# Performance work log

Hardware: AMD Instinct MI355X
Metric: run time of the kernel (lower is better)

Reference implementation:

```python
import jax, jax.numpy as jnp
import numpy as np

H, HD = 8, 64  # num_heads, head_dim
EPS = 1e-6

def rmsnorm(x, scale):
    return x * jax.lax.rsqrt(jnp.mean(x * x, axis=-1, keepdims=True) + EPS) * scale

def lecun(key, shape):
    fan_in = shape[0]
    return jax.random.normal(key, shape, dtype=jnp.float32) * (fan_in ** -0.5)

def setup_inputs() -> dict:
    key = jax.random.key(0)
    ks = jax.random.split(key, 12)
    B, S, D = 2, 512, 512
    hidden = H * HD            # 512
    ffn = 4 * D                # 2048
    return {
        "inputs": jax.random.normal(ks[0], (B, S, D), dtype=jnp.float32),
        "mask": jnp.zeros((B, S), dtype=jnp.float32),
        "carry": jnp.zeros((B, H, HD, HD), dtype=jnp.float32),
        "ln1": jnp.ones((D,), dtype=jnp.float32),
        "Wq": lecun(ks[1], (D, hidden)),
        "Wk": lecun(ks[2], (D, hidden)),
        "Wv": lecun(ks[3], (D, hidden)),
        "attn_ln": jnp.ones((hidden,), dtype=jnp.float32),
        "Wo": lecun(ks[4], (hidden, D)),
        "bo": jnp.zeros((D,), dtype=jnp.float32),
        "ln2": jnp.ones((D,), dtype=jnp.float32),
        "Wg": lecun(ks[5], (D, ffn)),
        "Wu": lecun(ks[6], (D, ffn)),
        "Wd": lecun(ks[7], (ffn, D)),
    }

def reference(inputs, mask, carry, ln1, Wq, Wk, Wv, attn_ln, Wo, bo, ln2, Wg, Wu, Wd):
    B, S, D = inputs.shape
    skip = inputs
    x = rmsnorm(inputs, ln1)
    # projections + relu feature map
    q = jax.nn.relu((x @ Wq).reshape(B, S, H, HD))
    k = jax.nn.relu((x @ Wk).reshape(B, S, H, HD))
    v = (x @ Wv).reshape(B, S, H, HD)
    # matrix-valued state update: Bmat_t = v_t k_t^T  [B,S,H,HD,HD]
    Bmat = v[..., :, None] * k[..., None, :]
    # decay: identity, zeroed where mask==1 (episode reset)
    m = mask[:, :, None, None, None]
    A = jnp.broadcast_to(jnp.eye(HD, dtype=x.dtype), Bmat.shape) * (1.0 - m)

    def binop(lhs, rhs):
        a_i, b_i = lhs
        a_j, b_j = rhs
        return jnp.matmul(a_i, a_j), jnp.matmul(b_i, a_j) + b_j

    cum_decay, hidden_states = jax.lax.associative_scan(binop, (A, Bmat), axis=1)
    # fold in incoming carry
    states = jnp.matmul(carry[:, None], cum_decay) + hidden_states  # [B,S,H,HD,HD]
    attn = jnp.matmul(states, q[..., None]).squeeze(-1).reshape(B, S, H * HD)
    attn = rmsnorm(attn, attn_ln)
    y = attn @ Wo + bo
    final_carry = states[:, -1]
    # residual + SwiGLU FFN
    x = y + skip
    skip2 = x
    x = rmsnorm(x, ln2)
    x = (jax.nn.silu(x @ Wg) * (x @ Wu)) @ Wd
    return (final_carry, x + skip2)
```

## Files before the change

kernel.cpp:

```cpp
#include <hip/hip_runtime.h>
#include <math.h>

typedef __bf16 bf16x8 __attribute__((ext_vector_type(8)));
typedef float  f32x4  __attribute__((ext_vector_type(4)));

constexpr int B_=2, S_=512, D_=512, H_=8, HD_=64, FFN_=2048, NC_=8;
constexpr float EPS_=1e-6f;

__device__ __forceinline__ __bf16 f2bf(float f){
    union{float f;unsigned u;}x; x.f=f;
    unsigned r=(x.u+0x7fffu+((x.u>>16)&1u))>>16;
    union{unsigned short s;__bf16 b;}y; y.s=(unsigned short)r; return y.b;
}
__device__ __forceinline__ float bf2f(unsigned short s){
    union{unsigned u;float f;}x; x.u=((unsigned)s)<<16; return x.f;
}
__device__ __forceinline__ void bf8_f32(uint4 p, float* o){
    unsigned w[4]={p.x,p.y,p.z,p.w};
#pragma unroll
    for(int i=0;i<4;i++){ o[2*i]=bf2f((unsigned short)(w[i]&0xffffu)); o[2*i+1]=bf2f((unsigned short)(w[i]>>16)); }
}
__device__ __forceinline__ f32x4 MF(bf16x8 a, bf16x8 b, f32x4 c){
    return __builtin_amdgcn_mfma_f32_16x16x32_bf16(a,b,c,0,0,0);
}
#define GLOAD16(g,l) __builtin_amdgcn_global_load_lds((__attribute__((address_space(1))) const void*)(g),(__attribute__((address_space(3))) void*)(l),16,0,0)

__device__ __forceinline__ void rowsq_atomic(float* accb, int row0, int lane, float p[4]){
#pragma unroll
    for(int r=0;r<4;r++){
        float v = p[r];
        v += __shfl_xor(v, 1, 64);
        v += __shfl_xor(v, 2, 64);
        v += __shfl_xor(v, 4, 64);
        v += __shfl_xor(v, 8, 64);
        if((lane&15)==0) atomicAdd(accb + row0 + r, v);
    }
}

__global__ __launch_bounds__(256) void prep_k(const float* __restrict__ Wg,
    const float* __restrict__ Wu, const float* __restrict__ Wd,
    const float* __restrict__ Wq, const float* __restrict__ Wk,
    const float* __restrict__ Wv, const float* __restrict__ Wo,
    __bf16* __restrict__ WT, const float* __restrict__ inputs,
    float* __restrict__ rs1, float* __restrict__ rs2acc, float* __restrict__ rs3acc){
    __shared__ __bf16 s[64][72];
    int t = blockIdx.x, tid = threadIdx.x;
    if(t >= 1024){
        int row = (t-1024)*4 + (tid>>6), lane = tid&63;
        const float4* p = (const float4*)(inputs + (size_t)row*D_) + lane*2;
        float4 a=p[0], b=p[1];
        float ss = a.x*a.x+a.y*a.y+a.z*a.z+a.w*a.w + b.x*b.x+b.y*b.y+b.z*b.z+b.w*b.w;
        for(int off=32; off>0; off>>=1) ss += __shfl_down(ss, off, 64);
        if(lane==0) rs1[row] = rsqrtf(ss/(float)D_ + EPS_);
        float4 z = {0.f,0.f,0.f,0.f};
        if(t==1024) ((float4*)rs2acc)[tid] = z;
        if(t==1025) ((float4*)rs3acc)[tid] = z;
        return;
    }
    const float* src; __bf16* dst; int K,N,lt;
    if      (t<256){ src=Wg; dst=WT;          K=512;  N=2048; lt=t; }
    else if (t<512){ src=Wu; dst=WT+1048576;  K=512;  N=2048; lt=t-256; }
    else if (t<768){ src=Wd; dst=WT+2097152;  K=2048; N=512;  lt=t-512; }
    else if (t<832){ src=Wq; dst=WT+3145728;  K=512;  N=512;  lt=t-768; }
    else if (t<896){ src=Wk; dst=WT+3407872;  K=512;  N=512;  lt=t-832; }
    else if (t<960){ src=Wv; dst=WT+3670016;  K=512;  N=512;  lt=t-896; }
    else           { src=Wo; dst=WT+3932160;  K=512;  N=512;  lt=t-960; }
    int nt64 = N>>6, tk = lt/nt64, tn = lt%nt64;
    {
        int jk = tid>>2, jn0 = (tid&3)*16;
        const float* p = src + (size_t)(tk*64+jk)*N + tn*64 + jn0;
        float4 a0=((const float4*)p)[0], a1=((const float4*)p)[1],
               a2=((const float4*)p)[2], a3=((const float4*)p)[3];
        bf16x8 w0, w1;
        w0[0]=f2bf(a0.x); w0[1]=f2bf(a0.y); w0[2]=f2bf(a0.z); w0[3]=f2bf(a0.w);
        w0[4]=f2bf(a1.x); w0[5]=f2bf(a1.y); w0[6]=f2bf(a1.z); w0[7]=f2bf(a1.w);
        w1[0]=f2bf(a2.x); w1[1]=f2bf(a2.y); w1[2]=f2bf(a2.z); w1[3]=f2bf(a2.w);
        w1[4]=f2bf(a3.x); w1[5]=f2bf(a3.y); w1[6]=f2bf(a3.z); w1[7]=f2bf(a3.w);
        *(bf16x8*)&s[jk][jn0] = w0; *(bf16x8*)&s[jk][jn0+8] = w1;
    }
    __syncthreads();
    {
        int jn = tid&63, jkq = (tid>>6)*16;
        bf16x8 w0, w1;
#pragma unroll
        for(int j=0;j<8;j++){ w0[j]=s[jkq+j][jn]; w1[j]=s[jkq+8+j][jn]; }
        __bf16* q = dst + (size_t)(tn*64+jn)*K + tk*64 + jkq;
        *(bf16x8*)q = w0; *(bf16x8*)(q+8) = w1;
    }
}

__device__ __forceinline__ void stageB1(const __bf16* __restrict__ Bt, int n0, int K, int kk,
                                        __bf16* sB0, __bf16* sB1, int wave, int lane){
    int row = (wave<<4) + (lane>>2), kq = (lane&3)<<3;
    const __bf16* g = Bt + (size_t)(n0+row)*K + kk + kq;
    GLOAD16(g,      sB0 + (wave<<9));
    GLOAD16(g + 32, sB1 + (wave<<9));
}
struct ARf { float4 a0,a1,a2,a3, g0,g1,g2,g3; };
__device__ __forceinline__ ARf loadA_f32(const float* __restrict__ A, const float* __restrict__ g,
                                         int m0, int K, int kk, int tid){
    int row = tid>>2, kq = (tid&3)<<4;
    const float4* p = (const float4*)(A + (size_t)(m0+row)*K + kk + kq);
    const float4* gp = (const float4*)(g + kk + kq);
    ARf o;
    o.a0=p[0]; o.a1=p[1]; o.a2=p[2]; o.a3=p[3];
    o.g0=gp[0]; o.g1=gp[1]; o.g2=gp[2]; o.g3=gp[3];
    return o;
}
__device__ __forceinline__ void writeA_f32(const ARf& o, float r, __bf16* sA0, __bf16* sA1, int tid){
    int row = tid>>2, kq = (tid&3)<<4;
    bf16x8 w0, w1;
    w0[0]=f2bf(o.a0.x*r*o.g0.x); w0[1]=f2bf(o.a0.y*r*o.g0.y);
    w0[2]=f2bf(o.a0.z*r*o.g0.z); w0[3]=f2bf(o.a0.w*r*o.g0.w);
    w0[4]=f2bf(o.a1.x*r*o.g1.x); w0[5]=f2bf(o.a1.y*r*o.g1.y);
    w0[6]=f2bf(o.a1.z*r*o.g1.z); w0[7]=f2bf(o.a1.w*r*o.g1.w);
    w1[0]=f2bf(o.a2.x*r*o.g2.x); w1[1]=f2bf(o.a2.y*r*o.g2.y);
    w1[2]=f2bf(o.a2.z*r*o.g2.z); w1[3]=f2bf(o.a2.w*r*o.g2.w);
    w1[4]=f2bf(o.a3.x*r*o.g3.x); w1[5]=f2bf(o.a3.y*r*o.g3.y);
    w1[6]=f2bf(o.a3.z*r*o.g3.z); w1[7]=f2bf(o.a3.w*r*o.g3.w);
    __bf16* d = (kq<32) ? (sA0 + row*32 + kq) : (sA1 + row*32 + kq-32);
    *(bf16x8*)d = w0; *(bf16x8*)(d+8) = w1;
}
struct ARb { uint4 p0,p1; float4 g0,g1,g2,g3; };
__device__ __forceinline__ ARb loadA_bf16(const __bf16* __restrict__ A, const float* __restrict__ g,
                                          int m0, int K, int kk, int tid){
    int row = tid>>2, kq = (tid&3)<<4;
    const __bf16* p = A + (size_t)(m0+row)*K + kk + kq;
    const float4* gp = (const float4*)(g + kk + kq);
    ARb o;
    o.p0 = *(const uint4*)p; o.p1 = *(const uint4*)(p+8);
    o.g0=gp[0]; o.g1=gp[1]; o.g2=gp[2]; o.g3=gp[3];
    return o;
}
__device__ __forceinline__ void writeA_bf16(const ARb& o, float r, __bf16* sA0, __bf16* sA1, int tid){
    int row = tid>>2, kq = (tid&3)<<4;
    float v[16]; bf8_f32(o.p0, v); bf8_f32(o.p1, v+8);
    float gf[16] = {o.g0.x,o.g0.y,o.g0.z,o.g0.w, o.g1.x,o.g1.y,o.g1.z,o.g1.w,
                    o.g2.x,o.g2.y,o.g2.z,o.g2.w, o.g3.x,o.g3.y,o.g3.z,o.g3.w};
    bf16x8 w0, w1;
#pragma unroll
    for(int j=0;j<8;j++){ w0[j]=f2bf(v[j]*r*gf[j]); w1[j]=f2bf(v[8+j]*r*gf[8+j]); }
    __bf16* d = (kq<32) ? (sA0 + row*32 + kq) : (sA1 + row*32 + kq-32);
    *(bf16x8*)d = w0; *(bf16x8*)(d+8) = w1;
}
__device__ __forceinline__ void mfma_tile(const __bf16* sA0, const __bf16* sA1,
        const __bf16* sB0, const __bf16* sB1, int wave, int lane, f32x4 acc[4]){
    int ar = (((wave<<4)+(lane&15))<<5) + ((lane>>4)<<3);
    bf16x8 a0 = *(const bf16x8*)(sA0+ar);
    bf16x8 a1 = *(const bf16x8*)(sA1+ar);
#pragma unroll
    for(int nt=0;nt<4;nt++){
        int br = (((nt<<4)+(lane&15))<<5) + ((lane>>4)<<3);
        acc[nt] = MF(a0, *(const bf16x8*)(sB0+br), acc[nt]);
        acc[nt] = MF(a1, *(const bf16x8*)(sB1+br), acc[nt]);
    }
}

__global__ __launch_bounds__(256) void gemm_qkv_k(const float* __restrict__ in,
        const float* __restrict__ rs1, const float* __restrict__ ln1,
        const __bf16* __restrict__ Bt, __bf16* __restrict__ Qb,
        __bf16* __restrict__ Kb, __bf16* __restrict__ Vb){
    __shared__ __bf16 sA0[2][2048], sA1[2][2048], sB0[2][2048], sB1[2][2048];
    int tid=threadIdx.x, wave=tid>>6, lane=tid&63;
    int n0 = blockIdx.x*64, m0 = blockIdx.y*64;
    float r = rs1[m0+(tid>>2)];
    f32x4 acc[4] = {};
    {
        ARf a = loadA_f32(in, ln1, m0, 512, 0, tid);
        stageB1(Bt, n0, 512, 0, sB0[0], sB1[0], wave, lane);
        writeA_f32(a, r, sA0[0], sA1[0], tid);
        __syncthreads();
    }
    int cur = 0;
#pragma unroll
    for(int it=0; it<8; ++it){
        int nxt = cur^1;
        ARf a;
        if(it<7){
            a = loadA_f32(in, ln1, m0, 512, (it+1)*64, tid);
            stageB1(Bt, n0, 512, (it+1)*64, sB0[nxt], sB1[nxt], wave, lane);
        }
        mfma_tile(sA0[cur],sA1[cur],sB0[cur],sB1[cur],wave,lane,acc);
        if(it<7) writeA_f32(a, r, sA0[nxt], sA1[nxt], tid);
        __syncthreads();
        cur = nxt;
    }
    int seg = n0>>9, nc = n0&511;
    __bf16* Out = seg==0 ? Qb : (seg==1 ? Kb : Vb);
    bool rl = seg<2;
    int r0 = (wave<<4) + ((lane>>4)<<2);
#pragma unroll
    for(int nt=0;nt<4;nt++){
        int col = nc + nt*16 + (lane&15);
#pragma unroll
        for(int rr=0;rr<4;rr++){
            float v = acc[nt][rr]; if(rl) v = fmaxf(v,0.f);
            Out[(size_t)(m0+r0+rr)*512 + col] = f2bf(v);
        }
    }
}

__global__ __launch_bounds__(256) void scanA_k(const __bf16* __restrict__ Kb,
        const __bf16* __restrict__ Vb, const float* __restrict__ mask,
        __bf16* __restrict__ MS, float* __restrict__ Pws){
    int bid = blockIdx.x;
    int c = bid&7, h = (bid>>3)&7, b = bid>>6;
    __shared__ __bf16 sKT0[2048], sKT1[2048], sVT0[2048], sVT1[2048];
    __shared__ float scv[64], ssp[64];
    int tid = threadIdx.x, wave = tid>>6, lane = tid&63;
    const __bf16* Kg = Kb + (size_t)(b*512 + c*64)*512 + h*64;
    const __bf16* Vg = Vb + (size_t)(b*512 + c*64)*512 + h*64;
    if(tid<64) scv[tid] = 1.f - mask[b*512 + c*64 + tid];
    __syncthreads();
    if(tid==0){
        float sp = 1.f;
        for(int t=63;t>=0;--t){ ssp[t]=sp; sp*=scv[t]; }
        Pws[bid] = sp;
    }
    __syncthreads();
#pragma unroll
    for(int p=0;p<2;p++){
        int t = (tid>>3) + p*32, i0 = (tid&7)*8;
        uint4 kr = *(const uint4*)(Kg + (size_t)t*512 + i0);
        uint4 vr = *(const uint4*)(Vg + (size_t)t*512 + i0);
        const __bf16* kp = (const __bf16*)&kr;
        const unsigned short* vp = (const unsigned short*)&vr;
        float sp = ssp[t];
        __bf16* kh = p ? sKT1 : sKT0;
        __bf16* vh = p ? sVT1 : sVT0;
#pragma unroll
        for(int j=0;j<8;j++){
            kh[(i0+j)*32 + (t&31)] = kp[j];
            vh[(i0+j)*32 + (t&31)] = f2bf(bf2f(vp[j])*sp);
        }
    }
    __syncthreads();
    f32x4 am[4] = {};
    mfma_tile(sVT0, sVT1, sKT0, sKT1, wave, lane, am);
    __bf16* Mo = MS + (size_t)bid*4096;
    int r0 = (wave<<4) + ((lane>>4)<<2);
#pragma unroll
    for(int nt=0;nt<4;nt++){
        int j = nt*16 + (lane&15);
#pragma unroll
        for(int r=0;r<4;r++) Mo[(size_t)(r0+r)*64 + j] = f2bf(am[nt][r]);
    }
}

__global__ __launch_bounds__(256) void scanC_k(const __bf16* __restrict__ Qb,
        const __bf16* __restrict__ Kb, const __bf16* __restrict__ Vb,
        const float* __restrict__ mask, const __bf16* __restrict__ MS,
        const float* __restrict__ carry, const float* __restrict__ Pws,
        float* __restrict__ carry_out, __bf16* __restrict__ attn,
        float* __restrict__ rs2acc){
    int bid = blockIdx.x;
    int c = bid&7, h = (bid>>3)&7, b = bid>>6;
    int bh = b*H_ + h;
    __shared__ __bf16 sQ0[2048], sQ1[2048], sK0[2048], sK1[2048];
    __shared__ __bf16 sS0[2048], sS1[2048];
    __shared__ __bf16 sVT0[2048], sVT1[2048];
    __shared__ __bf16 sW0[2048], sW1[2048];
    __shared__ float Wtab[64][64];
    __shared__ float scv[64], pp[64];
    int tid = threadIdx.x, wave = tid>>6, lane = tid&63;
    const __bf16* Qg = Qb + (size_t)(b*512 + c*64)*512 + h*64;
    const __bf16* Kg = Kb + (size_t)(b*512 + c*64)*512 + h*64;
    const __bf16* Vg = Vb + (size_t)(b*512 + c*64)*512 + h*64;

    stageB1(Qg, 0, 512, 0, sQ0, sQ1, wave, lane);
    stageB1(Kg, 0, 512, 0, sK0, sK1, wave, lane);
    if(tid<64) scv[tid] = 1.f - mask[b*512 + c*64 + tid];
#pragma unroll
    for(int p=0;p<2;p++){
        int u = (tid>>3) + p*32, i0 = (tid&7)*8;
        uint4 vr = *(const uint4*)(Vg + (size_t)u*512 + i0);
        const __bf16* vp = (const __bf16*)&vr;
        __bf16* vh = p ? sVT1 : sVT0;
#pragma unroll
        for(int j=0;j<8;j++) vh[(i0+j)*32 + (u&31)] = vp[j];
    }
    {
        int i = tid>>2, j0 = (tid&3)*16;
        float s[16];
        const float4* c4 = (const float4*)(carry + (size_t)bh*4096 + i*64 + j0);
        float4 s4[4] = {c4[0],c4[1],c4[2],c4[3]};
        float* sp = (float*)s4;
#pragma unroll
        for(int j=0;j<16;j++) s[j]=sp[j];
        for(int cc=0; cc<c; ++cc){
            float P = Pws[bh*8+cc];
            const __bf16* mp = MS + ((size_t)bh*8+cc)*4096 + i*64 + j0;
            float mv[16]; bf8_f32(*(const uint4*)mp, mv); bf8_f32(*(const uint4*)(mp+8), mv+8);
#pragma unroll
            for(int j=0;j<16;j++) s[j] = s[j]*P + mv[j];
        }
        bf16x8 w0, w1;
#pragma unroll
        for(int j=0;j<8;j++){ w0[j]=f2bf(s[j]); w1[j]=f2bf(s[8+j]); }
        __bf16* d = (j0<32) ? (sS0 + i*32 + j0) : (sS1 + i*32 + j0-32);
        *(bf16x8*)d = w0; *(bf16x8*)(d+8) = w1;
        if(c==7){
            float P = Pws[bh*8+7];
            const __bf16* mp = MS + ((size_t)bh*8+7)*4096 + i*64 + j0;
            float mv[16]; bf8_f32(*(const uint4*)mp, mv); bf8_f32(*(const uint4*)(mp+8), mv+8);
            float4 o4[4];
            float* ov = (float*)o4;
#pragma unroll
            for(int j=0;j<16;j++) ov[j] = s[j]*P + mv[j];
            float4* co = (float4*)(carry_out + (size_t)bh*4096 + i*64 + j0);
            co[0]=o4[0]; co[1]=o4[1]; co[2]=o4[2]; co[3]=o4[3];
        }
    }
    __syncthreads();
    if(tid<64){
        int u = tid; float w = 1.f;
        for(int t=0;t<64;t++){
            if(t>u) w *= scv[t];
            Wtab[u][t] = (t<u) ? 0.f : w;
        }
    }
    if(tid==64){
        float p=1.f;
        for(int t=0;t<64;t++){ p*=scv[t]; pp[t]=p; }
    }
    f32x4 sc[4] = {};
    mfma_tile(sK0, sK1, sQ0, sQ1, wave, lane, sc);
    __syncthreads();
    {
        int u0 = (wave<<4) + ((lane>>4)<<2);
#pragma unroll
        for(int nt=0;nt<4;nt++){
            int t = nt*16 + (lane&15);
#pragma unroll
            for(int r=0;r<4;r++){
                int u = u0 + r;
                float v = sc[nt][r] * Wtab[u][t];
                ((u<32) ? sW0 : sW1)[t*32 + (u&31)] = f2bf(v);
            }
        }
    }
    __syncthreads();
    f32x4 aI[4] = {}, aX[4] = {};
    mfma_tile(sW0, sW1, sVT0, sVT1, wave, lane, aI);
    mfma_tile(sQ0, sQ1, sS0, sS1, wave, lane, aX);
    int t0 = (wave<<4) + ((lane>>4)<<2);
    float psum[4] = {0.f,0.f,0.f,0.f};
#pragma unroll
    for(int nt=0;nt<4;nt++){
        int i = nt*16 + (lane&15);
#pragma unroll
        for(int r=0;r<4;r++){
            int t = t0 + r;
            float o = aI[nt][r] + aX[nt][r]*pp[t];
            attn[(size_t)(b*512 + c*64 + t)*512 + h*64 + i] = f2bf(o);
            psum[r] += o*o;
        }
    }
    rowsq_atomic(rs2acc, b*512 + c*64 + t0, lane, psum);
}

__global__ __launch_bounds__(256) void gemm_wo_k(const __bf16* __restrict__ attn,
        const float* __restrict__ rs2acc, const float* __restrict__ aln,
        const __bf16* __restrict__ Bt, const float* __restrict__ bo,
        const float* __restrict__ skip, float* __restrict__ outx,
        __bf16* __restrict__ X1, float* __restrict__ rs3acc){
    __shared__ __bf16 sA0[2][2048], sA1[2][2048], sB0[2][2048], sB1[2][2048];
    int tid=threadIdx.x, wave=tid>>6, lane=tid&63;
    int n0 = blockIdx.x*64, m0 = blockIdx.y*64;
    float r = rsqrtf(rs2acc[m0+(tid>>2)]*(1.f/(float)D_) + EPS_);
    f32x4 acc[4] = {};
    {
        ARb a = loadA_bf16(attn, aln, m0, 512, 0, tid);
        stageB1(Bt, n0, 512, 0, sB0[0], sB1[0], wave, lane);
        writeA_bf16(a, r, sA0[0], sA1[0], tid);
        __syncthreads();
    }
    int cur = 0;
#pragma unroll
    for(int it=0; it<8; ++it){
        int nxt = cur^1;
        ARb a;
        if(it<7){
            a = loadA_bf16(attn, aln, m0, 512, (it+1)*64, tid);
            stageB1(Bt, n0, 512, (it+1)*64, sB0[nxt], sB1[nxt], wave, lane);
        }
        mfma_tile(sA0[cur],sA1[cur],sB0[cur],sB1[cur],wave,lane,acc);
        if(it<7) writeA_bf16(a, r, sA0[nxt], sA1[nxt], tid);
        __syncthreads();
        cur = nxt;
    }
    int r0 = (wave<<4) + ((lane>>4)<<2);
    float psum[4] = {0.f,0.f,0.f,0.f};
#pragma unroll
    for(int nt=0;nt<4;nt++){
        int col = n0 + nt*16 + (lane&15);
#pragma unroll
        for(int rr=0;rr<4;rr++){
            int row = m0+r0+rr;
            float v = acc[nt][rr] + bo[col] + skip[(size_t)row*512+col];
            outx[(size_t)row*512+col] = v;
            X1[(size_t)row*512+col] = f2bf(v);
            psum[rr] += v*v;
        }
    }
    rowsq_atomic(rs3acc, m0+r0, lane, psum);
}

__global__ __launch_bounds__(256) void gemm_dual_k(const __bf16* __restrict__ X1,
        const float* __restrict__ rs3acc, const float* __restrict__ ln2,
        const __bf16* __restrict__ Gt, const __bf16* __restrict__ Ut,
        __bf16* __restrict__ Hb){
    __shared__ __bf16 sA0[2][2048], sA1[2][2048];
    __shared__ __bf16 sG0[2][2048], sG1[2][2048], sU0[2][2048], sU1[2][2048];
    int tid=threadIdx.x, wave=tid>>6, lane=tid&63;
    int n0 = blockIdx.x*64, m0 = blockIdx.y*64;
    float r = rsqrtf(rs3acc[m0+(tid>>2)]*(1.f/(float)D_) + EPS_);
    f32x4 ag[4] = {}, au[4] = {};
    {
        ARb a = loadA_bf16(X1, ln2, m0, 512, 0, tid);
        stageB1(Gt, n0, 512, 0, sG0[0], sG1[0], wave, lane);
        stageB1(Ut, n0, 512, 0, sU0[0], sU1[0], wave, lane);
        writeA_bf16(a, r, sA0[0], sA1[0], tid);
        __syncthreads();
    }
    int cur = 0;
#pragma unroll
    for(int it=0; it<8; ++it){
        int nxt = cur^1;
        ARb a;
        if(it<7){
            a = loadA_bf16(X1, ln2, m0, 512, (it+1)*64, tid);
            stageB1(Gt, n0, 512, (it+1)*64, sG0[nxt], sG1[nxt], wave, lane);
            stageB1(Ut, n0, 512, (it+1)*64, sU0[nxt], sU1[nxt], wave, lane);
        }
        {
            int ar = (((wave<<4)+(lane&15))<<5) + ((lane>>4)<<3);
            bf16x8 a0 = *(const bf16x8*)(sA0[cur]+ar);
            bf16x8 a1 = *(const bf16x8*)(sA1[cur]+ar);
#pragma unroll
            for(int nt=0;nt<4;nt++){
                int br = (((nt<<4)+(lane&15))<<5) + ((lane>>4)<<3);
                ag[nt] = MF(a0, *(const bf16x8*)(sG0[cur]+br), ag[nt]);
                ag[nt] = MF(a1, *(const bf16x8*)(sG1[cur]+br), ag[nt]);
                au[nt] = MF(a0, *(const bf16x8*)(sU0[cur]+br), au[nt]);
                au[nt] = MF(a1, *(const bf16x8*)(sU1[cur]+br), au[nt]);
            }
        }
        if(it<7) writeA_bf16(a, r, sA0[nxt], sA1[nxt], tid);
        __syncthreads();
        cur = nxt;
    }
    int r0 = (wave<<4) + ((lane>>4)<<2);
#pragma unroll
    for(int nt=0;nt<4;nt++){
        int col = n0 + nt*16 + (lane&15);
#pragma unroll
        for(int rr=0;rr<4;rr++){
            float gv = ag[nt][rr], uv = au[nt][rr];
            float hv = (gv / (1.f + __expf(-gv))) * uv;
            Hb[(size_t)(m0+r0+rr)*FFN_ + col] = f2bf(hv);
        }
    }
}

__global__ __launch_bounds__(256) void gemm_wd_k(const __bf16* __restrict__ Hb,
        const __bf16* __restrict__ Bt, float* __restrict__ outx){
    __shared__ __bf16 sA0[2][2048], sA1[2][2048], sB0[2][2048], sB1[2][2048];
    int tid=threadIdx.x, wave=tid>>6, lane=tid&63;
    int n0 = blockIdx.x*64, m0 = blockIdx.y*64, ks = blockIdx.z*512;
    f32x4 acc[4] = {};
    int row = (wave<<4) + (lane>>2), kq = (lane&3)<<3;
    {
        stageB1(Bt, n0, FFN_, ks, sB0[0], sB1[0], wave, lane);
        const __bf16* g = Hb + (size_t)(m0+row)*FFN_ + ks + kq;
        GLOAD16(g,      sA0[0] + (wave<<9));
        GLOAD16(g + 32, sA1[0] + (wave<<9));
        __syncthreads();
    }
    int cur = 0;
#pragma unroll
    for(int it=0; it<8; ++it){
        int nxt = cur^1;
        if(it<7){
            int kk = ks + (it+1)*64;
            stageB1(Bt, n0, FFN_, kk, sB0[nxt], sB1[nxt], wave, lane);
            const __bf16* g = Hb + (size_t)(m0+row)*FFN_ + kk + kq;
            GLOAD16(g,      sA0[nxt] + (wave<<9));
            GLOAD16(g + 32, sA1[nxt] + (wave<<9));
        }
        mfma_tile(sA0[cur],sA1[cur],sB0[cur],sB1[cur],wave,lane,acc);
        __syncthreads();
        cur = nxt;
    }
    int r0 = (wave<<4) + ((lane>>4)<<2);
#pragma unroll
    for(int nt=0;nt<4;nt++){
        int col = n0 + nt*16 + (lane&15);
#pragma unroll
        for(int r=0;r<4;r++)
            atomicAdd(&outx[(size_t)(m0+r0+r)*512 + col], acc[nt][r]);
    }
}

extern "C" void kernel_launch(void* const* d_in, const int* in_sizes, int n_in,
                              void* d_out, int out_size, void* d_ws, size_t ws_size,
                              hipStream_t stream) {
    const float* inputs  = (const float*)d_in[0];
    const float* mask    = (const float*)d_in[1];
    const float* carry   = (const float*)d_in[2];
    const float* ln1     = (const float*)d_in[3];
    const float* Wq      = (const float*)d_in[4];
    const float* Wk      = (const float*)d_in[5];
    const float* Wv      = (const float*)d_in[6];
    const float* attn_ln = (const float*)d_in[7];
    const float* Wo      = (const float*)d_in[8];
    const float* bo      = (const float*)d_in[9];
    const float* ln2     = (const float*)d_in[10];
    const float* Wg      = (const float*)d_in[11];
    const float* Wu      = (const float*)d_in[12];
    const float* Wd      = (const float*)d_in[13];

    float* out_carry = (float*)d_out;
    float* out_x     = (float*)d_out + 65536;

    __bf16* wb = (__bf16*)d_ws;
    float*  wf = (float*)d_ws;
    __bf16* WgT   = wb;
    __bf16* WuT   = wb + 1048576;
    __bf16* WdT   = wb + 2097152;
    __bf16* WqkvT = wb + 3145728;
    __bf16* WoT   = wb + 3932160;
    __bf16* Qb    = wb + 4194304;
    __bf16* Kb    = wb + 4718592;
    __bf16* Vb    = wb + 5242880;
    __bf16* Hb    = wb + 3145728;
    __bf16* MS    = wb + 5767168;
    float*  Pws   = wf + 3145728;
    float*  rs1   = wf + 3145856;
    float*  rs2a  = wf + 3146880;
    float*  rs3a  = wf + 3147904;

    prep_k<<<dim3(1280), dim3(256), 0, stream>>>(Wg,Wu,Wd,Wq,Wk,Wv,Wo, wb, inputs, rs1, rs2a, rs3a);
    gemm_qkv_k<<<dim3(24,16), dim3(256), 0, stream>>>(inputs, rs1, ln1, WqkvT, Qb, Kb, Vb);
    scanA_k<<<dim3(128), dim3(256), 0, stream>>>(Kb, Vb, mask, MS, Pws);
    scanC_k<<<dim3(128), dim3(256), 0, stream>>>(Qb, Kb, Vb, mask, MS, carry, Pws, out_carry, Qb, rs2a);
    gemm_wo_k<<<dim3(8,16), dim3(256), 0, stream>>>(Qb, rs2a, attn_ln, WoT, bo, inputs, out_x, Vb, rs3a);
    gemm_dual_k<<<dim3(32,16), dim3(256), 0, stream>>>(Vb, rs3a, ln2, WgT, WuT, Hb);
    gemm_wd_k<<<dim3(8,16,4), dim3(256), 0, stream>>>(Hb, WdT, out_x);
}
```

Before: 161.7 us.

## Fuse chunked scan into one sequential kernel, coalesce epilogue stores, drop split-K atomics

The two-pass chunked scan (per-chunk state kernel plus prefix kernel) is replaced by a single kernel with one block per batch-head that walks the 8 chunks in order and keeps the running state in registers. That removes a launch and the intermediate state buffer, but only 16 blocks run instead of 128. Several GEMM epilogues now stage results in shared memory and write coalesced 16-byte stores. The Wd GEMM drops its 4-way split-K with atomics for one 32-step K loop per tile, which gives fewer blocks and a longer serial loop.

```diff
diff --git a/kernel.cpp b/kernel.cpp
--- a/kernel.cpp
+++ b/kernel.cpp
@@ -188,175 +188,173 @@
     int seg = n0>>9, nc = n0&511;
     __bf16* Out = seg==0 ? Qb : (seg==1 ? Kb : Vb);
     bool rl = seg<2;
+    __bf16* tile = &sA0[0][0];
     int r0 = (wave<<4) + ((lane>>4)<<2);
 #pragma unroll
     for(int nt=0;nt<4;nt++){
-        int col = nc + nt*16 + (lane&15);
+        int col = nt*16 + (lane&15);
 #pragma unroll
         for(int rr=0;rr<4;rr++){
             float v = acc[nt][rr]; if(rl) v = fmaxf(v,0.f);
-            Out[(size_t)(m0+r0+rr)*512 + col] = f2bf(v);
-        }
-    }
-}
-
-__global__ __launch_bounds__(256) void scanA_k(const __bf16* __restrict__ Kb,
-        const __bf16* __restrict__ Vb, const float* __restrict__ mask,
-        __bf16* __restrict__ MS, float* __restrict__ Pws){
-    int bid = blockIdx.x;
-    int c = bid&7, h = (bid>>3)&7, b = bid>>6;
-    __shared__ __bf16 sKT0[2048], sKT1[2048], sVT0[2048], sVT1[2048];
-    __shared__ float scv[64], ssp[64];
-    int tid = threadIdx.x, wave = tid>>6, lane = tid&63;
-    const __bf16* Kg = Kb + (size_t)(b*512 + c*64)*512 + h*64;
-    const __bf16* Vg = Vb + (size_t)(b*512 + c*64)*512 + h*64;
-    if(tid<64) scv[tid] = 1.f - mask[b*512 + c*64 + tid];
-    __syncthreads();
-    if(tid==0){
-        float sp = 1.f;
-        for(int t=63;t>=0;--t){ ssp[t]=sp; sp*=scv[t]; }
-        Pws[bid] = sp;
+            tile[(r0+rr)*64 + col] = f2bf(v);
+        }
     }
     __syncthreads();
 #pragma unroll
     for(int p=0;p<2;p++){
-        int t = (tid>>3) + p*32, i0 = (tid&7)*8;
-        uint4 kr = *(const uint4*)(Kg + (size_t)t*512 + i0);
-        uint4 vr = *(const uint4*)(Vg + (size_t)t*512 + i0);
-        const __bf16* kp = (const __bf16*)&kr;
-        const unsigned short* vp = (const unsigned short*)&vr;
-        float sp = ssp[t];
-        __bf16* kh = p ? sKT1 : sKT0;
-        __bf16* vh = p ? sVT1 : sVT0;
-#pragma unroll
-        for(int j=0;j<8;j++){
-            kh[(i0+j)*32 + (t&31)] = kp[j];
-            vh[(i0+j)*32 + (t&31)] = f2bf(bf2f(vp[j])*sp);
-        }
-    }
-    __syncthreads();
-    f32x4 am[4] = {};
-    mfma_tile(sVT0, sVT1, sKT0, sKT1, wave, lane, am);
-    __bf16* Mo = MS + (size_t)bid*4096;
-    int r0 = (wave<<4) + ((lane>>4)<<2);
-#pragma unroll
-    for(int nt=0;nt<4;nt++){
-        int j = nt*16 + (lane&15);
-#pragma unroll
-        for(int r=0;r<4;r++) Mo[(size_t)(r0+r)*64 + j] = f2bf(am[nt][r]);
-    }
-}
-
-__global__ __launch_bounds__(256) void scanC_k(const __bf16* __restrict__ Qb,
+        int row = (tid>>3) + p*32, c0 = (tid&7)*8;
+        *(uint4*)(Out + (size_t)(m0+row)*512 + nc + c0) = *(const uint4*)&tile[row*64 + c0];
+    }
+}
+
+__global__ __launch_bounds__(256) void scan_k(const __bf16* __restrict__ Qb,
         const __bf16* __restrict__ Kb, const __bf16* __restrict__ Vb,
-        const float* __restrict__ mask, const __bf16* __restrict__ MS,
-        const float* __restrict__ carry, const float* __restrict__ Pws,
+        const float* __restrict__ mask, const float* __restrict__ carry,
         float* __restrict__ carry_out, __bf16* __restrict__ attn,
         float* __restrict__ rs2acc){
-    int bid = blockIdx.x;
-    int c = bid&7, h = (bid>>3)&7, b = bid>>6;
-    int bh = b*H_ + h;
-    __shared__ __bf16 sQ0[2048], sQ1[2048], sK0[2048], sK1[2048];
-    __shared__ __bf16 sS0[2048], sS1[2048];
-    __shared__ __bf16 sVT0[2048], sVT1[2048];
-    __shared__ __bf16 sW0[2048], sW1[2048];
+    int bh = blockIdx.x, h = bh & 7, b = bh >> 3;
+    __shared__ __bf16 sQ[4096], sK[4096], sKT[4096], sVT[4096], sS[4096], sW[4096];
     __shared__ float Wtab[64][64];
-    __shared__ float scv[64], pp[64];
+    __shared__ float scv[64], ssp[64], pp[64];
+    __shared__ float Psh;
     int tid = threadIdx.x, wave = tid>>6, lane = tid&63;
-    const __bf16* Qg = Qb + (size_t)(b*512 + c*64)*512 + h*64;
-    const __bf16* Kg = Kb + (size_t)(b*512 + c*64)*512 + h*64;
-    const __bf16* Vg = Vb + (size_t)(b*512 + c*64)*512 + h*64;
-
-    stageB1(Qg, 0, 512, 0, sQ0, sQ1, wave, lane);
-    stageB1(Kg, 0, 512, 0, sK0, sK1, wave, lane);
-    if(tid<64) scv[tid] = 1.f - mask[b*512 + c*64 + tid];
-#pragma unroll
-    for(int p=0;p<2;p++){
-        int u = (tid>>3) + p*32, i0 = (tid&7)*8;
-        uint4 vr = *(const uint4*)(Vg + (size_t)u*512 + i0);
-        const __bf16* vp = (const __bf16*)&vr;
-        __bf16* vh = p ? sVT1 : sVT0;
-#pragma unroll
-        for(int j=0;j<8;j++) vh[(i0+j)*32 + (u&31)] = vp[j];
-    }
-    {
-        int i = tid>>2, j0 = (tid&3)*16;
-        float s[16];
-        const float4* c4 = (const float4*)(carry + (size_t)bh*4096 + i*64 + j0);
-        float4 s4[4] = {c4[0],c4[1],c4[2],c4[3]};
-        float* sp = (float*)s4;
-#pragma unroll
-        for(int j=0;j<16;j++) s[j]=sp[j];
-        for(int cc=0; cc<c; ++cc){
-            float P = Pws[bh*8+cc];
-            const __bf16* mp = MS + ((size_t)bh*8+cc)*4096 + i*64 + j0;
-            float mv[16]; bf8_f32(*(const uint4*)mp, mv); bf8_f32(*(const uint4*)(mp+8), mv+8);
-#pragma unroll
-            for(int j=0;j<16;j++) s[j] = s[j]*P + mv[j];
-        }
-        bf16x8 w0, w1;
-#pragma unroll
-        for(int j=0;j<8;j++){ w0[j]=f2bf(s[j]); w1[j]=f2bf(s[8+j]); }
-        __bf16* d = (j0<32) ? (sS0 + i*32 + j0) : (sS1 + i*32 + j0-32);
-        *(bf16x8*)d = w0; *(bf16x8*)(d+8) = w1;
-        if(c==7){
-            float P = Pws[bh*8+7];
-            const __bf16* mp = MS + ((size_t)bh*8+7)*4096 + i*64 + j0;
-            float mv[16]; bf8_f32(*(const uint4*)mp, mv); bf8_f32(*(const uint4*)(mp+8), mv+8);
-            float4 o4[4];
-            float* ov = (float*)o4;
-#pragma unroll
-            for(int j=0;j<16;j++) ov[j] = s[j]*P + mv[j];
-            float4* co = (float4*)(carry_out + (size_t)bh*4096 + i*64 + j0);
-            co[0]=o4[0]; co[1]=o4[1]; co[2]=o4[2]; co[3]=o4[3];
-        }
-    }
-    __syncthreads();
-    if(tid<64){
-        int u = tid; float w = 1.f;
-        for(int t=0;t<64;t++){
-            if(t>u) w *= scv[t];
-            Wtab[u][t] = (t<u) ? 0.f : w;
-        }
-    }
-    if(tid==64){
-        float p=1.f;
-        for(int t=0;t<64;t++){ p*=scv[t]; pp[t]=p; }
-    }
-    f32x4 sc[4] = {};
-    mfma_tile(sK0, sK1, sQ0, sQ1, wave, lane, sc);
-    __syncthreads();
-    {
-        int u0 = (wave<<4) + ((lane>>4)<<2);
+    int r0 = (wave<<4) + ((lane>>4)<<2);
+    int jc = lane & 15;
+
+#pragma unroll
+    for(int p=0;p<4;p++){
+        int fi = tid + p*256;
+        int row = fi>>4, c4 = (fi&15)*4;
+        *(float4*)&Wtab[row][c4] = *(const float4*)(carry + (size_t)bh*4096 + row*64 + c4);
+    }
+    __syncthreads();
+    f32x4 S[4];
+#pragma unroll
+    for(int nt=0;nt<4;nt++)
+#pragma unroll
+        for(int rr=0;rr<4;rr++) S[nt][rr] = Wtab[r0+rr][nt*16+jc];
+    __syncthreads();
+
+    for(int c=0; c<NC_; ++c){
+        const __bf16* Qg = Qb + (size_t)(b*512 + c*64)*512 + h*64;
+        const __bf16* Kg = Kb + (size_t)(b*512 + c*64)*512 + h*64;
+        const __bf16* Vg = Vb + (size_t)(b*512 + c*64)*512 + h*64;
+        stageB1(Qg, 0, 512, 0, sQ, sQ+2048, wave, lane);
+        stageB1(Kg, 0, 512, 0, sK, sK+2048, wave, lane);
+        uint4 kv[2], vv[2];
+#pragma unroll
+        for(int p=0;p<2;p++){
+            int u = (tid>>3) + p*32, i0 = (tid&7)*8;
+            kv[p] = *(const uint4*)(Kg + (size_t)u*512 + i0);
+            vv[p] = *(const uint4*)(Vg + (size_t)u*512 + i0);
+        }
+        if(tid<64) scv[tid] = 1.f - mask[b*512 + c*64 + tid];
 #pragma unroll
         for(int nt=0;nt<4;nt++){
-            int t = nt*16 + (lane&15);
-#pragma unroll
-            for(int r=0;r<4;r++){
-                int u = u0 + r;
-                float v = sc[nt][r] * Wtab[u][t];
-                ((u<32) ? sW0 : sW1)[t*32 + (u&31)] = f2bf(v);
+            int j = nt*16 + jc;
+            __bf16* half = (j<32) ? sS : sS+2048;
+#pragma unroll
+            for(int rr=0;rr<4;rr++) half[(r0+rr)*32 + (j&31)] = f2bf(S[nt][rr]);
+        }
+        __syncthreads();
+        if(tid==0){
+            float sp=1.f;
+            for(int t=63;t>=0;--t){ ssp[t]=sp; sp*=scv[t]; }
+            Psh = sp;
+        }
+        if(tid==64){
+            float p=1.f;
+            for(int t=0;t<64;t++){ p*=scv[t]; pp[t]=p; }
+        }
+        if(tid<64){
+            int u=tid; float w=1.f;
+            for(int t=0;t<64;t++){ if(t>u) w*=scv[t]; Wtab[u][t]=(t<u)?0.f:w; }
+        }
+#pragma unroll
+        for(int p=0;p<2;p++){
+            int u = (tid>>3) + p*32, i0 = (tid&7)*8;
+            const __bf16* vp = (const __bf16*)&vv[p];
+            __bf16* vh = (i0<32)? sVT : sVT;
+#pragma unroll
+            for(int j=0;j<8;j++){
+                int i = i0+j;
+                ((i<32)? sVT : sVT+2048)[0];
+                ((u<32)? sVT : sVT+2048)[i*32 + (u&31)] = vp[j];
             }
         }
-    }
-    __syncthreads();
-    f32x4 aI[4] = {}, aX[4] = {};
-    mfma_tile(sW0, sW1, sVT0, sVT1, wave, lane, aI);
-    mfma_tile(sQ0, sQ1, sS0, sS1, wave, lane, aX);
-    int t0 = (wave<<4) + ((lane>>4)<<2);
-    float psum[4] = {0.f,0.f,0.f,0.f};
-#pragma unroll
-    for(int nt=0;nt<4;nt++){
-        int i = nt*16 + (lane&15);
-#pragma unroll
-        for(int r=0;r<4;r++){
-            int t = t0 + r;
-            float o = aI[nt][r] + aX[nt][r]*pp[t];
-            attn[(size_t)(b*512 + c*64 + t)*512 + h*64 + i] = f2bf(o);
-            psum[r] += o*o;
-        }
-    }
-    rowsq_atomic(rs2acc, b*512 + c*64 + t0, lane, psum);
+        __syncthreads();
+#pragma unroll
+        for(int p=0;p<2;p++){
+            int u = (tid>>3) + p*32, i0 = (tid&7)*8;
+            const unsigned short* kp = (const unsigned short*)&kv[p];
+            float sp = ssp[u];
+#pragma unroll
+            for(int j=0;j<8;j++){
+                int jj = i0+j;
+                ((u<32)? sKT : sKT+2048)[jj*32 + (u&31)] = f2bf(bf2f(kp[j])*sp);
+            }
+        }
+        __syncthreads();
+        f32x4 sc[4] = {}, aM[4] = {}, aX[4] = {};
+        mfma_tile(sK, sK+2048, sQ, sQ+2048, wave, lane, sc);
+        mfma_tile(sVT, sVT+2048, sKT, sKT+2048, wave, lane, aM);
+        mfma_tile(sQ, sQ+2048, sS, sS+2048, wave, lane, aX);
+#pragma unroll
+        for(int nt=0;nt<4;nt++){
+            int t = nt*16 + jc;
+#pragma unroll
+            for(int rr=0;rr<4;rr++){
+                int u = r0 + rr;
+                float v = sc[nt][rr] * Wtab[u][t];
+                ((u<32)? sW : sW+2048)[t*32 + (u&31)] = f2bf(v);
+            }
+        }
+        __syncthreads();
+        f32x4 aI[4] = {};
+        mfma_tile(sW, sW+2048, sVT, sVT+2048, wave, lane, aI);
+        float P = Psh;
+        float attv[4][4];
+        float psum[4] = {0.f,0.f,0.f,0.f};
+#pragma unroll
+        for(int nt=0;nt<4;nt++){
+#pragma unroll
+            for(int rr=0;rr<4;rr++){
+                int t = r0 + rr;
+                float o = aI[nt][rr] + aX[nt][rr]*pp[t];
+                attv[nt][rr] = o;
+                psum[rr] += o*o;
+                S[nt][rr] = S[nt][rr]*P + aM[nt][rr];
+            }
+        }
+        rowsq_atomic(rs2acc, b*512 + c*64 + r0, lane, psum);
+        __syncthreads();
+        __bf16* tile = sKT;
+#pragma unroll
+        for(int nt=0;nt<4;nt++){
+            int i = nt*16 + jc;
+#pragma unroll
+            for(int rr=0;rr<4;rr++) tile[(r0+rr)*64 + i] = f2bf(attv[nt][rr]);
+        }
+        __syncthreads();
+#pragma unroll
+        for(int p=0;p<2;p++){
+            int row = (tid>>3) + p*32, c0 = (tid&7)*8;
+            *(uint4*)(attn + (size_t)(b*512 + c*64 + row)*512 + h*64 + c0) =
+                *(const uint4*)&tile[row*64 + c0];
+        }
+        __syncthreads();
+    }
+#pragma unroll
+    for(int nt=0;nt<4;nt++)
+#pragma unroll
+        for(int rr=0;rr<4;rr++) Wtab[r0+rr][nt*16+jc] = S[nt][rr];
+    __syncthreads();
+#pragma unroll
+    for(int p=0;p<4;p++){
+        int fi = tid + p*256;
+        int row = fi>>4, c4 = (fi&15)*4;
+        *(float4*)(carry_out + (size_t)bh*4096 + row*64 + c4) = *(const float4*)&Wtab[row][c4];
+    }
 }
 
 __global__ __launch_bounds__(256) void gemm_wo_k(const __bf16* __restrict__ attn,
@@ -391,6 +389,7 @@
     }
     int r0 = (wave<<4) + ((lane>>4)<<2);
     float psum[4] = {0.f,0.f,0.f,0.f};
+    __bf16* tile = &sA0[0][0];
 #pragma unroll
     for(int nt=0;nt<4;nt++){
         int col = n0 + nt*16 + (lane&15);
@@ -399,11 +398,17 @@
             int row = m0+r0+rr;
             float v = acc[nt][rr] + bo[col] + skip[(size_t)row*512+col];
             outx[(size_t)row*512+col] = v;
-            X1[(size_t)row*512+col] = f2bf(v);
+            tile[(r0+rr)*64 + nt*16 + (lane&15)] = f2bf(v);
             psum[rr] += v*v;
         }
     }
     rowsq_atomic(rs3acc, m0+r0, lane, psum);
+    __syncthreads();
+#pragma unroll
+    for(int p=0;p<2;p++){
+        int row = (tid>>3) + p*32, c0 = (tid&7)*8;
+        *(uint4*)(X1 + (size_t)(m0+row)*512 + n0 + c0) = *(const uint4*)&tile[row*64 + c0];
+    }
 }
 
 __global__ __launch_bounds__(256) void gemm_dual_k(const __bf16* __restrict__ X1,
@@ -451,15 +456,22 @@
         cur = nxt;
     }
     int r0 = (wave<<4) + ((lane>>4)<<2);
+    __bf16* tile = &sA0[0][0];
 #pragma unroll
     for(int nt=0;nt<4;nt++){
-        int col = n0 + nt*16 + (lane&15);
+        int col = nt*16 + (lane&15);
 #pragma unroll
         for(int rr=0;rr<4;rr++){
             float gv = ag[nt][rr], uv = au[nt][rr];
             float hv = (gv / (1.f + __expf(-gv))) * uv;
-            Hb[(size_t)(m0+r0+rr)*FFN_ + col] = f2bf(hv);
-        }
+            tile[(r0+rr)*64 + col] = f2bf(hv);
+        }
+    }
+    __syncthreads();
+#pragma unroll
+    for(int p=0;p<2;p++){
+        int row = (tid>>3) + p*32, c0 = (tid&7)*8;
+        *(uint4*)(Hb + (size_t)(m0+row)*FFN_ + n0 + c0) = *(const uint4*)&tile[row*64 + c0];
     }
 }
 
@@ -467,22 +479,21 @@
         const __bf16* __restrict__ Bt, float* __restrict__ outx){
     __shared__ __bf16 sA0[2][2048], sA1[2][2048], sB0[2][2048], sB1[2][2048];
     int tid=threadIdx.x, wave=tid>>6, lane=tid&63;
-    int n0 = blockIdx.x*64, m0 = blockIdx.y*64, ks = blockIdx.z*512;
+    int n0 = blockIdx.x*64, m0 = blockIdx.y*64;
     f32x4 acc[4] = {};
     int row = (wave<<4) + (lane>>2), kq = (lane&3)<<3;
     {
-        stageB1(Bt, n0, FFN_, ks, sB0[0], sB1[0], wave, lane);
-        const __bf16* g = Hb + (size_t)(m0+row)*FFN_ + ks + kq;
+        stageB1(Bt, n0, FFN_, 0, sB0[0], sB1[0], wave, lane);
+        const __bf16* g = Hb + (size_t)(m0+row)*FFN_ + kq;
         GLOAD16(g,      sA0[0] + (wave<<9));
         GLOAD16(g + 32, sA1[0] + (wave<<9));
         __syncthreads();
     }
     int cur = 0;
-#pragma unroll
-    for(int it=0; it<8; ++it){
+    for(int it=0; it<32; ++it){
         int nxt = cur^1;
-        if(it<7){
-            int kk = ks + (it+1)*64;
+        if(it<31){
+            int kk = (it+1)*64;
             stageB1(Bt, n0, FFN_, kk, sB0[nxt], sB1[nxt], wave, lane);
             const __bf16* g = Hb + (size_t)(m0+row)*FFN_ + kk + kq;
             GLOAD16(g,      sA0[nxt] + (wave<<9));
@@ -497,8 +508,10 @@
     for(int nt=0;nt<4;nt++){
         int col = n0 + nt*16 + (lane&15);
 #pragma unroll
-        for(int r=0;r<4;r++)
-            atomicAdd(&outx[(size_t)(m0+r0+r)*512 + col], acc[nt][r]);
+        for(int rr=0;rr<4;rr++){
+            size_t idx = (size_t)(m0+r0+rr)*512 + col;
+            outx[idx] = outx[idx] + acc[nt][rr];
+        }
     }
 }
 
@@ -534,17 +547,14 @@
     __bf16* Kb    = wb + 4718592;
     __bf16* Vb    = wb + 5242880;
     __bf16* Hb    = wb + 3145728;
-    __bf16* MS    = wb + 5767168;
-    float*  Pws   = wf + 3145728;
     float*  rs1   = wf + 3145856;
     float*  rs2a  = wf + 3146880;
     float*  rs3a  = wf + 3147904;
 
     prep_k<<<dim3(1280), dim3(256), 0, stream>>>(Wg,Wu,Wd,Wq,Wk,Wv,Wo, wb, inputs, rs1, rs2a, rs3a);
     gemm_qkv_k<<<dim3(24,16), dim3(256), 0, stream>>>(inputs, rs1, ln1, WqkvT, Qb, Kb, Vb);
-    scanA_k<<<dim3(128), dim3(256), 0, stream>>>(Kb, Vb, mask, MS, Pws);
-    scanC_k<<<dim3(128), dim3(256), 0, stream>>>(Qb, Kb, Vb, mask, MS, carry, Pws, out_carry, Qb, rs2a);
+    scan_k<<<dim3(16), dim3(256), 0, stream>>>(Qb, Kb, Vb, mask, carry, out_carry, Qb, rs2a);
     gemm_wo_k<<<dim3(8,16), dim3(256), 0, stream>>>(Qb, rs2a, attn_ln, WoT, bo, inputs, out_x, Vb, rs3a);
     gemm_dual_k<<<dim3(32,16), dim3(256), 0, stream>>>(Vb, rs3a, ln2, WgT, WuT, Hb);
-    gemm_wd_k<<<dim3(8,16,4), dim3(256), 0, stream>>>(Hb, WdT, out_x);
-}
+    gemm_wd_k<<<dim3(8,16), dim3(256), 0, stream>>>(Hb, WdT, out_x);
+}
```

After: 214.9 us. 1.33x slower.
